# Kernel tuning notes

Hardware: AMD Instinct MI355X
Metric: run time of the kernel (lower is better)

Reference implementation:

```python
import jax, jax.numpy as jnp
import numpy as np

N_NODES = 100000
N_EDGES = 3200000
D_FEAT = 512
HIDDEN = 16
N_CLASSES = 7


def setup_inputs() -> dict:
    key = jax.random.key(0)
    k1, k2, k3, k4 = jax.random.split(key, 4)
    x = jax.random.normal(k1, (N_NODES, D_FEAT), dtype=jnp.float32)
    edge_index = jax.random.randint(k2, (2, N_EDGES), 0, N_NODES, dtype=jnp.int64)
    # Glorot-ish scaled weights
    W1 = jax.random.normal(k3, (D_FEAT, HIDDEN), dtype=jnp.float32) * (1.0 / np.sqrt(D_FEAT))
    b1 = jnp.zeros((HIDDEN,), dtype=jnp.float32)
    W2 = jax.random.normal(k4, (HIDDEN, N_CLASSES), dtype=jnp.float32) * (1.0 / np.sqrt(HIDDEN))
    b2 = jnp.zeros((N_CLASSES,), dtype=jnp.float32)
    return {"x": x, "edge_index": edge_index, "W1": W1, "b1": b1, "W2": W2, "b2": b2}


def _gcn_norm(edge_index, num_nodes):
    # Add self-loops, then symmetric normalization: D^-1/2 A D^-1/2
    loop = jnp.arange(num_nodes, dtype=edge_index.dtype)
    src = jnp.concatenate([edge_index[0], loop])
    dst = jnp.concatenate([edge_index[1], loop])
    deg = jax.ops.segment_sum(jnp.ones_like(dst, dtype=jnp.float32), dst,
                              num_segments=num_nodes)
    dinv = jnp.where(deg > 0, jax.lax.rsqrt(deg), 0.0)
    w = dinv[src] * dinv[dst]  # [E+N]
    return src, dst, w


def _gcn_conv(x, W, b, src, dst, w, num_nodes):
    h = x @ W                               # transform first (small out dim)
    m = jax.ops.segment_sum(h[src] * w[:, None], dst, num_segments=num_nodes)
    return m + b


def reference(x, edge_index, W1, b1, W2, b2):
    n = x.shape[0]
    src, dst, w = _gcn_norm(edge_index, n)
    h = jax.nn.relu(_gcn_conv(x, W1, b1, src, dst, w, n))
    # dropout is identity at inference
    logits = _gcn_conv(h, W2, b2, src, dst, w, n)
    return jax.nn.log_softmax(logits, axis=1)
```

## Files before the change

### kernel.cpp

```cpp
#include <hip/hip_runtime.h>
#include <cmath>

#define N_NODES   100000
#define N_EDGES   3200000
#define D_FEAT    512
#define HIDDEN    16
#define N_CLASSES 7

#define NCHUNK 250
#define CHUNK  12800
#define NBKT   1563
#define NSCAN  (NBKT * NCHUNK)

typedef __attribute__((ext_vector_type(4))) float  f32x4;
typedef __attribute__((ext_vector_type(8))) short  bf16x8;

__device__ __forceinline__ short f2bf(float f) {
    union { float f; unsigned u; } v; v.f = f;
    unsigned r = v.u + 0x7fffu + ((v.u >> 16) & 1u);
    return (short)(r >> 16);
}
__device__ __forceinline__ float bf2f(unsigned short s) {
    union { unsigned u; float f; } v; v.u = ((unsigned)s) << 16;
    return v.f;
}

__global__ __launch_bounds__(1024) void k_hist1(const int* __restrict__ dst,
                                                unsigned* __restrict__ hist) {
    __shared__ unsigned h[NBKT];
    int t = threadIdx.x, b = blockIdx.x;
    for (int i = t; i < NBKT; i += 1024) h[i] = 0u;
    __syncthreads();
    int base = b * CHUNK;
    #pragma unroll 2
    for (int k = 0; k < 13; ++k) {
        int idx = k * 1024 + t;
        if (idx < CHUNK) atomicAdd(&h[((unsigned)dst[base + idx]) >> 6], 1u);
    }
    __syncthreads();
    for (int i = t; i < NBKT; i += 1024)
        hist[(size_t)i * NCHUNK + b] = h[i];
}

__global__ __launch_bounds__(256) void k_scan_a(unsigned* __restrict__ hist,
                                                unsigned* __restrict__ bin_total) {
    __shared__ unsigned t0[256];
    int t = threadIdx.x, b = blockIdx.x;
    unsigned v = (t < NCHUNK) ? hist[(size_t)b * NCHUNK + t] : 0u;
    t0[t] = v; __syncthreads();
    #pragma unroll
    for (int off = 1; off < 256; off <<= 1) {
        unsigned add = (t >= off) ? t0[t - off] : 0u;
        __syncthreads();
        t0[t] += add;
        __syncthreads();
    }
    if (t < NCHUNK) hist[(size_t)b * NCHUNK + t] = t0[t] - v;
    if (t == 255) bin_total[b] = t0[t];
}

__global__ __launch_bounds__(256) void k_scan_b(const unsigned* __restrict__ bin_total,
                                                unsigned* __restrict__ bin_base) {
    __shared__ unsigned t0[256];
    int t = threadIdx.x;
    unsigned running = 0u;
    for (int c0 = 0; c0 < NBKT; c0 += 256) {
        int i = c0 + t;
        unsigned v = (i < NBKT) ? bin_total[i] : 0u;
        t0[t] = v; __syncthreads();
        #pragma unroll
        for (int off = 1; off < 256; off <<= 1) {
            unsigned add = (t >= off) ? t0[t - off] : 0u;
            __syncthreads();
            t0[t] += add;
            __syncthreads();
        }
        if (i < NBKT) bin_base[i] = running + t0[t] - v;
        unsigned chunk_sum = t0[255];
        __syncthreads();
        running += chunk_sum;
    }
    if (t == 0) bin_base[NBKT] = running;
}

__global__ __launch_bounds__(1024) void k_scatter1(const int* __restrict__ src,
                                                   const int* __restrict__ dst,
                                                   const unsigned* __restrict__ hist,
                                                   const unsigned* __restrict__ bin_base,
                                                   unsigned* __restrict__ packed) {
    __shared__ unsigned cur[NBKT];
    int t = threadIdx.x, b = blockIdx.x;
    for (int i = t; i < NBKT; i += 1024)
        cur[i] = hist[(size_t)i * NCHUNK + b] + bin_base[i];
    __syncthreads();
    int base = b * CHUNK;
    #pragma unroll 2
    for (int k = 0; k < 13; ++k) {
        int idx = k * 1024 + t;
        if (idx < CHUNK) {
            int e = base + idx;
            unsigned d = (unsigned)dst[e];
            unsigned pos = atomicAdd(&cur[d >> 6], 1u);
            packed[pos] = ((d & 63u) << 24) | (unsigned)src[e];
        }
    }
}

__global__ __launch_bounds__(256) void k_bucket(const unsigned* __restrict__ packed,
                                                const unsigned* __restrict__ bin_base,
                                                unsigned* __restrict__ deg,
                                                unsigned* __restrict__ row_start,
                                                float* __restrict__ dinv,
                                                int* __restrict__ csr_src) {
    __shared__ unsigned hh[4][64], sc[64], cur[64];
    int t = threadIdx.x, b = blockIdx.x;
    int w = t >> 6, l = t & 63;
    unsigned rs = bin_base[b];
    unsigned re = bin_base[b + 1];
    hh[w][l] = 0u;
    __syncthreads();
    for (unsigned i = rs + t; i < re; i += 256)
        atomicAdd(&hh[w][packed[i] >> 24], 1u);
    __syncthreads();
    unsigned total = 0u;
    if (t < 64) {
        total = hh[0][t] + hh[1][t] + hh[2][t] + hh[3][t];
        sc[t] = total;
    }
    __syncthreads();
    #pragma unroll
    for (int off = 1; off < 64; off <<= 1) {
        unsigned add = (t >= off && t < 64) ? sc[t - off] : 0u;
        __syncthreads();
        if (t < 64) sc[t] += add;
        __syncthreads();
    }
    if (t < 64) {
        unsigned excl = sc[t] - total;
        int node = b * 64 + t;
        if (node < N_NODES) {
            deg[node]       = total;
            row_start[node] = rs + excl;
            dinv[node]      = rsqrtf((float)(total + 1u));
        }
        cur[t] = rs + excl;
    }
    __syncthreads();
    for (unsigned i = rs + t; i < re; i += 256) {
        unsigned p = packed[i];
        unsigned pos = atomicAdd(&cur[p >> 24], 1u);
        csr_src[pos] = (int)(p & 0xFFFFFFu);
    }
}

__global__ __launch_bounds__(256) void k_gemm1(const float* __restrict__ x,
                                               const float* __restrict__ w1,
                                               const float* __restrict__ dinv,
                                               unsigned short* __restrict__ h1p) {
    __shared__ __align__(16) short w1t[16][520];
    int tid = threadIdx.x;
    for (int idx = tid; idx < D_FEAT * HIDDEN; idx += 256) {
        int k = idx >> 4, n = idx & 15;
        w1t[n][k] = f2bf(w1[idx]);
    }
    __syncthreads();

    int lane = tid & 63, wid = tid >> 6;
    int m  = lane & 15;
    int kg = lane >> 4;

    bf16x8 bfrag[16];
    #pragma unroll
    for (int ks = 0; ks < 16; ++ks)
        bfrag[ks] = *(const bf16x8*)&w1t[m][ks * 32 + kg * 8];

    int tile = blockIdx.x * 4 + wid;
    if (tile >= (N_NODES / 16)) return;

    const f32x4* xr = (const f32x4*)(x + (size_t)(tile * 16 + m) * D_FEAT);
    f32x4 acc = {0.f, 0.f, 0.f, 0.f};
    #pragma unroll
    for (int ks = 0; ks < 16; ++ks) {
        f32x4 x0 = xr[ks * 8 + kg * 2];
        f32x4 x1 = xr[ks * 8 + kg * 2 + 1];
        bf16x8 a;
        a[0] = f2bf(x0[0]); a[1] = f2bf(x0[1]); a[2] = f2bf(x0[2]); a[3] = f2bf(x0[3]);
        a[4] = f2bf(x1[0]); a[5] = f2bf(x1[1]); a[6] = f2bf(x1[2]); a[7] = f2bf(x1[3]);
        acc = __builtin_amdgcn_mfma_f32_16x16x32_bf16(a, bfrag[ks], acc, 0, 0, 0);
    }
    size_t base = (size_t)tile * 256;
    #pragma unroll
    for (int r = 0; r < 4; ++r) {
        int rr = kg * 4 + r;
        h1p[base + rr * 16 + m] = (unsigned short)f2bf(dinv[tile * 16 + rr] * acc[r]);
    }
}

__global__ __launch_bounds__(256) void k_gather1(const int* __restrict__ csr_src,
                                                 const unsigned* __restrict__ row_start,
                                                 const unsigned* __restrict__ deg,
                                                 const unsigned short* __restrict__ h1p,
                                                 float* __restrict__ g1) {
    int tid  = threadIdx.x;
    int lane = tid & 63;
    int node = blockIdx.x * 4 + (tid >> 6);
    int j  = lane & 15;
    int sl = lane >> 4;

    unsigned start = row_start[node];
    unsigned end   = start + deg[node];

    float acc = (sl == 0) ? bf2f(h1p[(size_t)node * 16 + j]) : 0.f;
    unsigned e = start;
    for (; e + 16 <= end; e += 16) {
        int s0 = csr_src[e      + sl];
        int s1 = csr_src[e + 4  + sl];
        int s2 = csr_src[e + 8  + sl];
        int s3 = csr_src[e + 12 + sl];
        float v0 = bf2f(h1p[(size_t)s0 * 16 + j]);
        float v1 = bf2f(h1p[(size_t)s1 * 16 + j]);
        float v2 = bf2f(h1p[(size_t)s2 * 16 + j]);
        float v3 = bf2f(h1p[(size_t)s3 * 16 + j]);
        acc += v0; acc += v1; acc += v2; acc += v3;
    }
    for (; e < end; e += 4) {
        unsigned idx = e + (unsigned)sl;
        float v = 0.f;
        if (idx < end) v = bf2f(h1p[(size_t)csr_src[idx] * 16 + j]);
        acc += v;
    }
    acc += __shfl_down(acc, 32);
    acc += __shfl_down(acc, 16);
    if (sl == 0) g1[(size_t)node * 16 + j] = acc;
}

__global__ __launch_bounds__(256) void k_layer2(const float* __restrict__ g1,
                                                const float* __restrict__ dinv,
                                                const float* __restrict__ w2,
                                                const float* __restrict__ b1,
                                                float* __restrict__ h2p) {
    int i = blockIdx.x * 256 + threadIdx.x;
    if (i >= N_NODES) return;
    float di = dinv[i];
    const float* gr = g1 + (size_t)i * 16;
    float h[16];
    #pragma unroll
    for (int j = 0; j < 16; ++j) h[j] = fmaxf(di * gr[j] + b1[j], 0.f);
    float* h2r = h2p + (size_t)i * 8;
    #pragma unroll
    for (int c = 0; c < N_CLASSES; ++c) {
        float o = 0.f;
        #pragma unroll
        for (int j = 0; j < 16; ++j) o += h[j] * w2[j * N_CLASSES + c];
        h2r[c] = di * o;
    }
    h2r[7] = 0.f;
}

__global__ __launch_bounds__(256) void k_gather2(const int* __restrict__ csr_src,
                                                 const unsigned* __restrict__ row_start,
                                                 const unsigned* __restrict__ deg,
                                                 const float* __restrict__ dinv,
                                                 const float* __restrict__ h2p,
                                                 const float* __restrict__ b2,
                                                 float* __restrict__ out) {
    int tid  = threadIdx.x;
    int lane = tid & 63;
    int node = blockIdx.x * 4 + (tid >> 6);
    int j  = lane & 7;
    int sl = lane >> 3;

    unsigned start = row_start[node];
    unsigned end   = start + deg[node];

    float acc = (sl == 0) ? h2p[(size_t)node * 8 + j] : 0.f;
    unsigned e = start;
    for (; e + 32 <= end; e += 32) {
        int s0 = csr_src[e      + sl];
        int s1 = csr_src[e + 8  + sl];
        int s2 = csr_src[e + 16 + sl];
        int s3 = csr_src[e + 24 + sl];
        float v0 = h2p[(size_t)s0 * 8 + j];
        float v1 = h2p[(size_t)s1 * 8 + j];
        float v2 = h2p[(size_t)s2 * 8 + j];
        float v3 = h2p[(size_t)s3 * 8 + j];
        acc += v0; acc += v1; acc += v2; acc += v3;
    }
    for (; e < end; e += 8) {
        unsigned idx = e + (unsigned)sl;
        float v = 0.f;
        if (idx < end) v = h2p[(size_t)csr_src[idx] * 8 + j];
        acc += v;
    }
    acc += __shfl_down(acc, 32);
    acc += __shfl_down(acc, 16);
    acc += __shfl_down(acc, 8);
    float di = dinv[node];
    float logit = (j < N_CLASSES) ? di * acc + b2[j] : -1e30f;
    float mx = logit;
    #pragma unroll
    for (int mk = 1; mk < 8; mk <<= 1) mx = fmaxf(mx, __shfl_xor(mx, mk, 8));
    float ex = (j < N_CLASSES) ? __expf(logit - mx) : 0.f;
    float sum = ex;
    #pragma unroll
    for (int mk = 1; mk < 8; mk <<= 1) sum += __shfl_xor(sum, mk, 8);
    if (sl == 0 && j < N_CLASSES)
        out[(size_t)node * N_CLASSES + j] = logit - mx - __logf(sum);
}

extern "C" void kernel_launch(void* const* d_in, const int* in_sizes, int n_in,
                              void* d_out, int out_size, void* d_ws, size_t ws_size,
                              hipStream_t stream) {
    const float* x  = (const float*)d_in[0];
    const int*   ei = (const int*)d_in[1];
    const float* w1 = (const float*)d_in[2];
    const float* b1 = (const float*)d_in[3];
    const float* w2 = (const float*)d_in[4];
    const float* b2 = (const float*)d_in[5];
    float* out = (float*)d_out;

    const int* src = ei;
    const int* dst = ei + N_EDGES;

    unsigned* w32        = (unsigned*)d_ws;
    float*    dinv       = (float*)(w32 + 0);
    unsigned short* h1p  = (unsigned short*)(w32 + 102400);
    float*    g1         = (float*)(w32 + 902400);
    float*    h2p        = (float*)(w32 + 2502400);
    unsigned* deg        = w32 + 3302400;
    unsigned* row_start  = w32 + 3404800;
    unsigned* hist       = w32 + 3507200;
    unsigned* bin_total  = w32 + 3897984;
    unsigned* bin_base   = w32 + 3899552;
    unsigned* packed     = w32 + 3901120;
    int*      csr_src    = (int*)(w32 + 7101120);

    const int GB = (N_NODES / 16 + 3) / 4;

    k_hist1   <<<NCHUNK, 1024, 0, stream>>>(dst, hist);
    k_scan_a  <<<NBKT,   256,  0, stream>>>(hist, bin_total);
    k_scan_b  <<<1,      256,  0, stream>>>(bin_total, bin_base);
    k_scatter1<<<NCHUNK, 1024, 0, stream>>>(src, dst, hist, bin_base, packed);
    k_bucket  <<<NBKT,   256,  0, stream>>>(packed, bin_base, deg, row_start, dinv, csr_src);
    k_gemm1   <<<GB,     256,  0, stream>>>(x, w1, dinv, h1p);
    k_gather1 <<<25000,  256,  0, stream>>>(csr_src, row_start, deg, h1p, g1);
    k_layer2  <<<(N_NODES + 255) / 256, 256, 0, stream>>>(g1, dinv, w2, b1, h2p);
    k_gather2 <<<25000,  256,  0, stream>>>(csr_src, row_start, deg, dinv, h2p, b2, out);
}
```

Baseline: 490.1 us.

## Replace per-chunk histogram scan with global atomics; fuse layer2 into gather1

The bucket sort drops the per-chunk histogram matrix and its two-level scan. Each chunk now atomically adds its counts into a global bucket total, a single small scan produces bases and cursors, and the scatter kernel recomputes its local histogram and reserves ranges with global atomics. The layer-2 transform (bias, ReLU, 16x7 matmul, dinv scaling) is also fused into the end of gather1 using shuffles and shared W2, which removes the g1 round trip and one launch. The price is edge ordering within a bucket that now depends on atomic arrival order, so summation order is nondeterministic, plus an extra zeroing kernel and a repeated histogram pass in scatter.

```diff
diff --git a/kernel.cpp b/kernel.cpp
--- a/kernel.cpp
+++ b/kernel.cpp
@@ -10,7 +10,6 @@
 #define NCHUNK 250
 #define CHUNK  12800
 #define NBKT   1563
-#define NSCAN  (NBKT * NCHUNK)
 
 typedef __attribute__((ext_vector_type(4))) float  f32x4;
 typedef __attribute__((ext_vector_type(8))) short  bf16x8;
@@ -25,8 +24,13 @@
     return v.f;
 }
 
-__global__ __launch_bounds__(1024) void k_hist1(const int* __restrict__ dst,
-                                                unsigned* __restrict__ hist) {
+__global__ __launch_bounds__(256) void k_zero(unsigned* __restrict__ p, int n) {
+    int i = blockIdx.x * 256 + threadIdx.x;
+    if (i < n) p[i] = 0u;
+}
+
+__global__ __launch_bounds__(1024) void k_hist(const int* __restrict__ dst,
+                                               unsigned* __restrict__ bucket_count) {
     __shared__ unsigned h[NBKT];
     int t = threadIdx.x, b = blockIdx.x;
     for (int i = t; i < NBKT; i += 1024) h[i] = 0u;
@@ -38,35 +42,21 @@
         if (idx < CHUNK) atomicAdd(&h[((unsigned)dst[base + idx]) >> 6], 1u);
     }
     __syncthreads();
-    for (int i = t; i < NBKT; i += 1024)
-        hist[(size_t)i * NCHUNK + b] = h[i];
-}
-
-__global__ __launch_bounds__(256) void k_scan_a(unsigned* __restrict__ hist,
-                                                unsigned* __restrict__ bin_total) {
-    __shared__ unsigned t0[256];
-    int t = threadIdx.x, b = blockIdx.x;
-    unsigned v = (t < NCHUNK) ? hist[(size_t)b * NCHUNK + t] : 0u;
-    t0[t] = v; __syncthreads();
-    #pragma unroll
-    for (int off = 1; off < 256; off <<= 1) {
-        unsigned add = (t >= off) ? t0[t - off] : 0u;
-        __syncthreads();
-        t0[t] += add;
-        __syncthreads();
-    }
-    if (t < NCHUNK) hist[(size_t)b * NCHUNK + t] = t0[t] - v;
-    if (t == 255) bin_total[b] = t0[t];
-}
-
-__global__ __launch_bounds__(256) void k_scan_b(const unsigned* __restrict__ bin_total,
-                                                unsigned* __restrict__ bin_base) {
+    for (int i = t; i < NBKT; i += 1024) {
+        unsigned v = h[i];
+        if (v) atomicAdd(&bucket_count[i], v);
+    }
+}
+
+__global__ __launch_bounds__(256) void k_scan(const unsigned* __restrict__ bucket_count,
+                                              unsigned* __restrict__ bin_base,
+                                              unsigned* __restrict__ bin_cursor) {
     __shared__ unsigned t0[256];
     int t = threadIdx.x;
     unsigned running = 0u;
     for (int c0 = 0; c0 < NBKT; c0 += 256) {
         int i = c0 + t;
-        unsigned v = (i < NBKT) ? bin_total[i] : 0u;
+        unsigned v = (i < NBKT) ? bucket_count[i] : 0u;
         t0[t] = v; __syncthreads();
         #pragma unroll
         for (int off = 1; off < 256; off <<= 1) {
@@ -75,7 +65,11 @@
             t0[t] += add;
             __syncthreads();
         }
-        if (i < NBKT) bin_base[i] = running + t0[t] - v;
+        if (i < NBKT) {
+            unsigned e = running + t0[t] - v;
+            bin_base[i]   = e;
+            bin_cursor[i] = e;
+        }
         unsigned chunk_sum = t0[255];
         __syncthreads();
         running += chunk_sum;
@@ -83,24 +77,33 @@
     if (t == 0) bin_base[NBKT] = running;
 }
 
-__global__ __launch_bounds__(1024) void k_scatter1(const int* __restrict__ src,
-                                                   const int* __restrict__ dst,
-                                                   const unsigned* __restrict__ hist,
-                                                   const unsigned* __restrict__ bin_base,
-                                                   unsigned* __restrict__ packed) {
-    __shared__ unsigned cur[NBKT];
+__global__ __launch_bounds__(1024) void k_scatter(const int* __restrict__ src,
+                                                  const int* __restrict__ dst,
+                                                  unsigned* __restrict__ bin_cursor,
+                                                  unsigned* __restrict__ packed) {
+    __shared__ unsigned h[NBKT];
     int t = threadIdx.x, b = blockIdx.x;
-    for (int i = t; i < NBKT; i += 1024)
-        cur[i] = hist[(size_t)i * NCHUNK + b] + bin_base[i];
+    for (int i = t; i < NBKT; i += 1024) h[i] = 0u;
     __syncthreads();
     int base = b * CHUNK;
+    #pragma unroll 2
+    for (int k = 0; k < 13; ++k) {
+        int idx = k * 1024 + t;
+        if (idx < CHUNK) atomicAdd(&h[((unsigned)dst[base + idx]) >> 6], 1u);
+    }
+    __syncthreads();
+    for (int i = t; i < NBKT; i += 1024) {
+        unsigned c = h[i];
+        h[i] = c ? atomicAdd(&bin_cursor[i], c) : 0u;
+    }
+    __syncthreads();
     #pragma unroll 2
     for (int k = 0; k < 13; ++k) {
         int idx = k * 1024 + t;
         if (idx < CHUNK) {
             int e = base + idx;
             unsigned d = (unsigned)dst[e];
-            unsigned pos = atomicAdd(&cur[d >> 6], 1u);
+            unsigned pos = atomicAdd(&h[d >> 6], 1u);
             packed[pos] = ((d & 63u) << 24) | (unsigned)src[e];
         }
     }
@@ -200,8 +203,20 @@
                                                  const unsigned* __restrict__ row_start,
                                                  const unsigned* __restrict__ deg,
                                                  const unsigned short* __restrict__ h1p,
-                                                 float* __restrict__ g1) {
+                                                 const float* __restrict__ dinv,
+                                                 const float* __restrict__ w2,
+                                                 const float* __restrict__ b1,
+                                                 float* __restrict__ h2p) {
+    __shared__ float w2s[16][8];
+    __shared__ float b1s[16];
     int tid  = threadIdx.x;
+    if (tid < 128) {
+        int jj = tid >> 3, c = tid & 7;
+        w2s[jj][c] = (c < N_CLASSES) ? w2[jj * N_CLASSES + c] : 0.f;
+    }
+    if (tid < 16) b1s[tid] = b1[tid];
+    __syncthreads();
+
     int lane = tid & 63;
     int node = blockIdx.x * 4 + (tid >> 6);
     int j  = lane & 15;
@@ -231,30 +246,16 @@
     }
     acc += __shfl_down(acc, 32);
     acc += __shfl_down(acc, 16);
-    if (sl == 0) g1[(size_t)node * 16 + j] = acc;
-}
-
-__global__ __launch_bounds__(256) void k_layer2(const float* __restrict__ g1,
-                                                const float* __restrict__ dinv,
-                                                const float* __restrict__ w2,
-                                                const float* __restrict__ b1,
-                                                float* __restrict__ h2p) {
-    int i = blockIdx.x * 256 + threadIdx.x;
-    if (i >= N_NODES) return;
-    float di = dinv[i];
-    const float* gr = g1 + (size_t)i * 16;
-    float h[16];
-    #pragma unroll
-    for (int j = 0; j < 16; ++j) h[j] = fmaxf(di * gr[j] + b1[j], 0.f);
-    float* h2r = h2p + (size_t)i * 8;
-    #pragma unroll
-    for (int c = 0; c < N_CLASSES; ++c) {
-        float o = 0.f;
-        #pragma unroll
-        for (int j = 0; j < 16; ++j) o += h[j] * w2[j * N_CLASSES + c];
-        h2r[c] = di * o;
-    }
-    h2r[7] = 0.f;
+
+    float di = dinv[node];
+    float hv = fmaxf(fmaf(di, acc, b1s[j]), 0.f);
+    float o = 0.f;
+    int c = lane & 7;
+    #pragma unroll
+    for (int jj = 0; jj < 16; ++jj)
+        o = fmaf(__shfl(hv, jj), w2s[jj][c], o);
+    if (lane < 8)
+        h2p[(size_t)node * 8 + c] = (c < N_CLASSES) ? di * o : 0.f;
 }
 
 __global__ __launch_bounds__(256) void k_gather2(const int* __restrict__ csr_src,
@@ -322,28 +323,26 @@
     const int* src = ei;
     const int* dst = ei + N_EDGES;
 
-    unsigned* w32        = (unsigned*)d_ws;
-    float*    dinv       = (float*)(w32 + 0);
-    unsigned short* h1p  = (unsigned short*)(w32 + 102400);
-    float*    g1         = (float*)(w32 + 902400);
-    float*    h2p        = (float*)(w32 + 2502400);
-    unsigned* deg        = w32 + 3302400;
-    unsigned* row_start  = w32 + 3404800;
-    unsigned* hist       = w32 + 3507200;
-    unsigned* bin_total  = w32 + 3897984;
-    unsigned* bin_base   = w32 + 3899552;
-    unsigned* packed     = w32 + 3901120;
-    int*      csr_src    = (int*)(w32 + 7101120);
+    unsigned* w32            = (unsigned*)d_ws;
+    float*    dinv           = (float*)(w32 + 0);
+    unsigned short* h1p      = (unsigned short*)(w32 + 102400);
+    float*    h2p            = (float*)(w32 + 902400);
+    unsigned* deg            = w32 + 1702400;
+    unsigned* row_start      = w32 + 1804800;
+    unsigned* bucket_count   = w32 + 1907200;
+    unsigned* bin_base       = w32 + 1909248;
+    unsigned* bin_cursor     = w32 + 1911296;
+    unsigned* packed         = w32 + 1913344;
+    int*      csr_src        = (int*)(w32 + 5113344);
 
     const int GB = (N_NODES / 16 + 3) / 4;
 
-    k_hist1   <<<NCHUNK, 1024, 0, stream>>>(dst, hist);
-    k_scan_a  <<<NBKT,   256,  0, stream>>>(hist, bin_total);
-    k_scan_b  <<<1,      256,  0, stream>>>(bin_total, bin_base);
-    k_scatter1<<<NCHUNK, 1024, 0, stream>>>(src, dst, hist, bin_base, packed);
+    k_zero    <<<(NBKT + 255) / 256, 256, 0, stream>>>(bucket_count, NBKT);
+    k_hist    <<<NCHUNK, 1024, 0, stream>>>(dst, bucket_count);
+    k_scan    <<<1,      256,  0, stream>>>(bucket_count, bin_base, bin_cursor);
+    k_scatter <<<NCHUNK, 1024, 0, stream>>>(src, dst, bin_cursor, packed);
     k_bucket  <<<NBKT,   256,  0, stream>>>(packed, bin_base, deg, row_start, dinv, csr_src);
     k_gemm1   <<<GB,     256,  0, stream>>>(x, w1, dinv, h1p);
-    k_gather1 <<<25000,  256,  0, stream>>>(csr_src, row_start, deg, h1p, g1);
-    k_layer2  <<<(N_NODES + 255) / 256, 256, 0, stream>>>(g1, dinv, w2, b1, h2p);
+    k_gather1 <<<25000,  256,  0, stream>>>(csr_src, row_start, deg, h1p, dinv, w2, b1, h2p);
     k_gather2 <<<25000,  256,  0, stream>>>(csr_src, row_start, deg, dinv, h2p, b2, out);
 }
```

Measured after the change: 497.4 us. About the same (+1.5%).
